# Performance work log

Hardware: AMD Instinct MI355X
Metric: run time of the kernel (lower is better)

Reference implementation:

```python
import jax, jax.numpy as jnp
import numpy as np

D_K = 64  # key/query head dim used for the 1/sqrt(d_k) scale


def setup_inputs() -> dict:
    key0 = jax.random.key(0)
    kk, kq, kv = jax.random.split(key0, 3)
    B, H, S, DK, DV = 2, 16, 2048, 64, 64
    return {
        "key": jax.random.normal(kk, (B, H, S, DK), dtype=jnp.float32),
        "query": jax.random.normal(kq, (B, H, S, DK), dtype=jnp.float32),
        "value": jax.random.normal(kv, (B, H, S, DV), dtype=jnp.float32),
    }


def reference(key, query, value):
    # scaled dot-product attention per head: [B,H,S,S]
    scores = jnp.einsum("bhqd,bhkd->bhqk", query, key) / jnp.sqrt(jnp.asarray(D_K, query.dtype))
    attn = jax.nn.softmax(scores, axis=-1)
    out = jnp.einsum("bhqk,bhkv->bhqv", attn, value)  # [B,H,S,d_v]
    B, H, S, DV = out.shape
    # faithful to the torch .view: raw reshape (no head transpose)
    return out.reshape(B, S, H * DV)
```

## Files before the change

kernel.cpp:

```cpp
#include <hip/hip_runtime.h>

#define S_LEN 2048
#define DHEAD 64
#define BHEADS 32
#define NTILES 32
#define HEAD_ELEMS (S_LEN * DHEAD)
#define TENS_ELEMS (BHEADS * HEAD_ELEMS)
#define TILE_HALVES 4096

typedef _Float16 half8_t __attribute__((ext_vector_type(8)));
typedef _Float16 half4_t __attribute__((ext_vector_type(4)));
typedef _Float16 half2_t __attribute__((ext_vector_type(2)));
typedef float float4_t __attribute__((ext_vector_type(4)));

#define SC_LOG2E 0.18033688011112042f


__global__ __launch_bounds__(256) void prep_kernel(const float* __restrict__ K,
                                                   const float* __restrict__ V,
                                                   _Float16* __restrict__ Kf,
                                                   _Float16* __restrict__ Vf) {
    __shared__ _Float16 tile[64][72];
    const int bh = blockIdx.x >> 5;
    const int t = blockIdx.x & 31;
    const int tid = threadIdx.x;

    const float* Ksrc = K + (bh * S_LEN + t * 64) * DHEAD;
    const float4* vs = (const float4*)(V + (bh * S_LEN + t * 64) * DHEAD);
#pragma unroll
    for (int it = 0; it < 4; ++it) {
        int i = it * 256 + tid;
        float4 vv = vs[i];
        int r = i >> 4, c4 = (i & 15) * 4;
        half4_t hv = {(_Float16)vv.x, (_Float16)vv.y, (_Float16)vv.z, (_Float16)vv.w};
        *(half4_t*)&tile[r][c4] = hv;
    }

    _Float16* kd = Kf + (bh * NTILES + t) * TILE_HALVES;
#pragma unroll
    for (int it = 0; it < 2; ++it) {
        int c = it * 256 + tid;
        int f = c >> 6, lane = c & 63;
        int row = (f >> 1) * 16 + (lane & 15);
        int d0 = (f & 1) * 32 + (lane >> 4) * 8;
        const float4* s = (const float4*)(Ksrc + row * DHEAD + d0);
        float4 a = s[0], b = s[1];
        half8_t h = {(_Float16)(a.x * SC_LOG2E), (_Float16)(a.y * SC_LOG2E),
                     (_Float16)(a.z * SC_LOG2E), (_Float16)(a.w * SC_LOG2E),
                     (_Float16)(b.x * SC_LOG2E), (_Float16)(b.y * SC_LOG2E),
                     (_Float16)(b.z * SC_LOG2E), (_Float16)(b.w * SC_LOG2E)};
        *(half8_t*)(kd + c * 8) = h;
    }
    __syncthreads();

    _Float16* vd = Vf + (bh * NTILES + t) * TILE_HALVES;
#pragma unroll
    for (int it = 0; it < 2; ++it) {
        int c = it * 256 + tid;
        int fv = c >> 6, lane = c & 63;
        int vt = fv >> 1, ktp = fv & 1;
        int v = vt * 16 + (lane & 15);
        int g = lane >> 4;
        half8_t h;
#pragma unroll
        for (int j = 0; j < 8; ++j) {
            int key = ktp * 32 + (j >> 2) * 16 + g * 4 + (j & 3);
            h[j] = tile[key][v];
        }
        *(half8_t*)(vd + c * 8) = h;
    }
}


__global__ __launch_bounds__(256, 2) void attn_kernel(
    const float* __restrict__ Qf,
    const _Float16* __restrict__ Kf,
    const _Float16* __restrict__ Vf,
    float* __restrict__ out) {
    __shared__ float red[2][68][64];

    const int tid = threadIdx.x;
    const int wid = tid >> 6;
    const int lane = tid & 63;
    const int ln15 = lane & 15;
    const int g = lane >> 4;

    const int bh = blockIdx.x & 31;
    const int qidx = blockIdx.x >> 5;
    const int qg = wid >> 1;
    const int ks = wid & 1;
    const int q0 = qidx * 128 + qg * 64;
    const int t0 = ks * 16;

    const float* Qg = Qf + (bh * S_LEN + q0) * DHEAD;
    half8_t qf[4][2];
#pragma unroll
    for (int nq = 0; nq < 4; ++nq)
#pragma unroll
        for (int kh = 0; kh < 2; ++kh) {
            const float4* qs = (const float4*)(Qg + (nq * 16 + ln15) * DHEAD + kh * 32 + g * 8);
            float4 a = qs[0], b = qs[1];
            qf[nq][kh] = (half8_t){(_Float16)a.x, (_Float16)a.y, (_Float16)a.z, (_Float16)a.w,
                                   (_Float16)b.x, (_Float16)b.y, (_Float16)b.z, (_Float16)b.w};
        }

    const _Float16* kb = Kf + bh * (NTILES * TILE_HALVES) + t0 * TILE_HALVES;
    const _Float16* vb = Vf + bh * (NTILES * TILE_HALVES) + t0 * TILE_HALVES;
    const int lo = lane * 8;

    const half8_t vones = {(_Float16)1.f, (_Float16)1.f, (_Float16)1.f, (_Float16)1.f,
                           (_Float16)1.f, (_Float16)1.f, (_Float16)1.f, (_Float16)1.f};

    float4_t o[4][4];
    float4_t o4[4];
#pragma unroll
    for (int nq = 0; nq < 4; ++nq) {
#pragma unroll
        for (int vt = 0; vt < 4; ++vt) o[nq][vt] = (float4_t){0.f, 0.f, 0.f, 0.f};
        o4[nq] = (float4_t){0.f, 0.f, 0.f, 0.f};
    }

#pragma unroll 2
    for (int t = 0; t < 16; ++t) {
        const int base = t * TILE_HALVES;
        half8_t kf[8], vf[8];
#pragma unroll
        for (int f = 0; f < 8; ++f) kf[f] = *(const half8_t*)(kb + base + f * 512 + lo);
#pragma unroll
        for (int f = 0; f < 8; ++f) vf[f] = *(const half8_t*)(vb + base + f * 512 + lo);

#pragma unroll
        for (int c = 0; c < 2; ++c) {
            half8_t pb[4];
#pragma unroll
            for (int h = 0; h < 2; ++h) {
                const int mt = 2 * c + h;
                half8_t a0 = kf[mt * 2];
                half8_t a1 = kf[mt * 2 + 1];
#pragma unroll
                for (int nq = 0; nq < 4; ++nq) {
                    float4_t c0 = (float4_t){0.f, 0.f, 0.f, 0.f};
                    c0 = __builtin_amdgcn_mfma_f32_16x16x32_f16(a0, qf[nq][0], c0, 0, 0, 0);
                    c0 = __builtin_amdgcn_mfma_f32_16x16x32_f16(a1, qf[nq][1], c0, 0, 0, 0);
                    float p0 = __builtin_amdgcn_exp2f(c0[0]);
                    float p1 = __builtin_amdgcn_exp2f(c0[1]);
                    float p2 = __builtin_amdgcn_exp2f(c0[2]);
                    float p3 = __builtin_amdgcn_exp2f(c0[3]);
                    half2_t plo = __builtin_bit_cast(half2_t, __builtin_amdgcn_cvt_pkrtz(p0, p1));
                    half2_t phi = __builtin_bit_cast(half2_t, __builtin_amdgcn_cvt_pkrtz(p2, p3));
                    pb[nq][h * 4 + 0] = plo[0];
                    pb[nq][h * 4 + 1] = plo[1];
                    pb[nq][h * 4 + 2] = phi[0];
                    pb[nq][h * 4 + 3] = phi[1];
                }
            }
#pragma unroll
            for (int vt = 0; vt < 4; ++vt) {
                half8_t va = vf[vt * 2 + c];
#pragma unroll
                for (int nq = 0; nq < 4; ++nq)
                    o[nq][vt] = __builtin_amdgcn_mfma_f32_16x16x32_f16(va, pb[nq], o[nq][vt], 0, 0, 0);
            }
#pragma unroll
            for (int nq = 0; nq < 4; ++nq)
                o4[nq] = __builtin_amdgcn_mfma_f32_16x16x32_f16(vones, pb[nq], o4[nq], 0, 0, 0);
        }
    }

    float lsum[4];
#pragma unroll
    for (int nq = 0; nq < 4; ++nq) lsum[nq] = o4[nq][0];

    if (ks == 1) {
#pragma unroll
        for (int nq = 0; nq < 4; ++nq)
#pragma unroll
            for (int vt = 0; vt < 4; ++vt)
#pragma unroll
                for (int r = 0; r < 4; ++r)
                    red[qg][nq * 16 + vt * 4 + r][lane] = o[nq][vt][r];
#pragma unroll
        for (int nq = 0; nq < 4; ++nq) red[qg][64 + nq][lane] = lsum[nq];
    }
    __syncthreads();
    if (ks == 0) {
#pragma unroll
        for (int nq = 0; nq < 4; ++nq) {
            float lt = lsum[nq] + red[qg][64 + nq][lane];
            float inv_l = 1.0f / lt;
            int qg_global = q0 + nq * 16 + ln15;
            float* og = out + (bh * S_LEN + qg_global) * DHEAD;
#pragma unroll
            for (int vt = 0; vt < 4; ++vt) {
                float4_t vals;
#pragma unroll
                for (int r = 0; r < 4; ++r)
                    vals[r] = (o[nq][vt][r] + red[qg][nq * 16 + vt * 4 + r][lane]) * inv_l;
                *(float4_t*)(og + vt * 16 + g * 4) = vals;
            }
        }
    }
}


extern "C" void kernel_launch(void* const* d_in, const int* in_sizes, int n_in,
                              void* d_out, int out_size, void* d_ws, size_t ws_size,
                              hipStream_t stream) {
    const float* Kin = (const float*)d_in[0];
    const float* Qin = (const float*)d_in[1];
    const float* Vin = (const float*)d_in[2];
    float* out = (float*)d_out;

    _Float16* Kf = (_Float16*)d_ws;
    _Float16* Vf = Kf + TENS_ELEMS;

    prep_kernel<<<BHEADS * NTILES, 256, 0, stream>>>(Kin, Vin, Kf, Vf);
    attn_kernel<<<BHEADS * 16, 256, 0, stream>>>(Qin, Kf, Vf, out);
}
```

Baseline: 125.8 us.

## Split key range across three waves per 64-query block and load K/V per half-tile

Each block now handles 64 queries with three waves that split the 32 key tiles 11/11/10, instead of two query groups times two key halves. The grid doubles to 1024 blocks of 192 threads, and the per-wave partial outputs and row sums are reduced through shared memory by wave 0. K/V fragments are loaded per 32-key half inside the inner loop rather than all 16 up front, which cuts register pressure to allow three blocks per CU. The wave split is uneven, so one wave does less work, and the shared-memory reduction now combines two partials instead of one.

```diff
diff --git a/kernel.cpp b/kernel.cpp
--- a/kernel.cpp
+++ b/kernel.cpp
@@ -72,7 +72,7 @@
 }
 
 
-__global__ __launch_bounds__(256, 2) void attn_kernel(
+__global__ __launch_bounds__(192, 3) void attn_kernel(
     const float* __restrict__ Qf,
     const _Float16* __restrict__ Kf,
     const _Float16* __restrict__ Vf,
@@ -87,10 +87,10 @@
 
     const int bh = blockIdx.x & 31;
     const int qidx = blockIdx.x >> 5;
-    const int qg = wid >> 1;
-    const int ks = wid & 1;
-    const int q0 = qidx * 128 + qg * 64;
-    const int t0 = ks * 16;
+    const int ks = wid;
+    const int q0 = qidx * 64;
+    const int tstart = ks * 11;
+    const int tend = (ks == 2) ? 32 : (tstart + 11);
 
     const float* Qg = Qf + (bh * S_LEN + q0) * DHEAD;
     half8_t qf[4][2];
@@ -104,9 +104,10 @@
                                    (_Float16)b.x, (_Float16)b.y, (_Float16)b.z, (_Float16)b.w};
         }
 
-    const _Float16* kb = Kf + bh * (NTILES * TILE_HALVES) + t0 * TILE_HALVES;
-    const _Float16* vb = Vf + bh * (NTILES * TILE_HALVES) + t0 * TILE_HALVES;
+    const _Float16* kb = Kf + bh * (NTILES * TILE_HALVES) + tstart * TILE_HALVES;
+    const _Float16* vb = Vf + bh * (NTILES * TILE_HALVES) + tstart * TILE_HALVES;
     const int lo = lane * 8;
+    const int ntile = tend - tstart;
 
     const half8_t vones = {(_Float16)1.f, (_Float16)1.f, (_Float16)1.f, (_Float16)1.f,
                            (_Float16)1.f, (_Float16)1.f, (_Float16)1.f, (_Float16)1.f};
@@ -121,22 +122,24 @@
     }
 
 #pragma unroll 2
-    for (int t = 0; t < 16; ++t) {
+    for (int t = 0; t < ntile; ++t) {
         const int base = t * TILE_HALVES;
-        half8_t kf[8], vf[8];
-#pragma unroll
-        for (int f = 0; f < 8; ++f) kf[f] = *(const half8_t*)(kb + base + f * 512 + lo);
-#pragma unroll
-        for (int f = 0; f < 8; ++f) vf[f] = *(const half8_t*)(vb + base + f * 512 + lo);
 
 #pragma unroll
         for (int c = 0; c < 2; ++c) {
+            half8_t kA[4], vA[4];
+#pragma unroll
+            for (int i = 0; i < 4; ++i)
+                kA[i] = *(const half8_t*)(kb + base + (4 * c + i) * 512 + lo);
+#pragma unroll
+            for (int vt = 0; vt < 4; ++vt)
+                vA[vt] = *(const half8_t*)(vb + base + (vt * 2 + c) * 512 + lo);
+
             half8_t pb[4];
 #pragma unroll
             for (int h = 0; h < 2; ++h) {
-                const int mt = 2 * c + h;
-                half8_t a0 = kf[mt * 2];
-                half8_t a1 = kf[mt * 2 + 1];
+                half8_t a0 = kA[h * 2];
+                half8_t a1 = kA[h * 2 + 1];
 #pragma unroll
                 for (int nq = 0; nq < 4; ++nq) {
                     float4_t c0 = (float4_t){0.f, 0.f, 0.f, 0.f};
@@ -156,7 +159,7 @@
             }
 #pragma unroll
             for (int vt = 0; vt < 4; ++vt) {
-                half8_t va = vf[vt * 2 + c];
+                half8_t va = vA[vt];
 #pragma unroll
                 for (int nq = 0; nq < 4; ++nq)
                     o[nq][vt] = __builtin_amdgcn_mfma_f32_16x16x32_f16(va, pb[nq], o[nq][vt], 0, 0, 0);
@@ -171,22 +174,22 @@
 #pragma unroll
     for (int nq = 0; nq < 4; ++nq) lsum[nq] = o4[nq][0];
 
-    if (ks == 1) {
+    if (ks >= 1) {
 #pragma unroll
         for (int nq = 0; nq < 4; ++nq)
 #pragma unroll
             for (int vt = 0; vt < 4; ++vt)
 #pragma unroll
                 for (int r = 0; r < 4; ++r)
-                    red[qg][nq * 16 + vt * 4 + r][lane] = o[nq][vt][r];
-#pragma unroll
-        for (int nq = 0; nq < 4; ++nq) red[qg][64 + nq][lane] = lsum[nq];
+                    red[ks - 1][nq * 16 + vt * 4 + r][lane] = o[nq][vt][r];
+#pragma unroll
+        for (int nq = 0; nq < 4; ++nq) red[ks - 1][64 + nq][lane] = lsum[nq];
     }
     __syncthreads();
     if (ks == 0) {
 #pragma unroll
         for (int nq = 0; nq < 4; ++nq) {
-            float lt = lsum[nq] + red[qg][64 + nq][lane];
+            float lt = lsum[nq] + red[0][64 + nq][lane] + red[1][64 + nq][lane];
             float inv_l = 1.0f / lt;
             int qg_global = q0 + nq * 16 + ln15;
             float* og = out + (bh * S_LEN + qg_global) * DHEAD;
@@ -195,7 +198,8 @@
                 float4_t vals;
 #pragma unroll
                 for (int r = 0; r < 4; ++r)
-                    vals[r] = (o[nq][vt][r] + red[qg][nq * 16 + vt * 4 + r][lane]) * inv_l;
+                    vals[r] = (o[nq][vt][r] + red[0][nq * 16 + vt * 4 + r][lane]
+                                            + red[1][nq * 16 + vt * 4 + r][lane]) * inv_l;
                 *(float4_t*)(og + vt * 16 + g * 4) = vals;
             }
         }
@@ -215,5 +219,5 @@
     _Float16* Vf = Kf + TENS_ELEMS;
 
     prep_kernel<<<BHEADS * NTILES, 256, 0, stream>>>(Kin, Vin, Kf, Vf);
-    attn_kernel<<<BHEADS * 16, 256, 0, stream>>>(Qin, Kf, Vf, out);
+    attn_kernel<<<BHEADS * 32, 192, 0, stream>>>(Qin, Kf, Vf, out);
 }
```

Result: no change. 126.5 us (+0.5%).
